# Kernel optimization log

Measured on AMD Instinct MI355X. Metric: run time of the kernel, lower is better.

Reference implementation:

```python
import jax, jax.numpy as jnp
import numpy as np
from math import sqrt

DIM = 64
N_HEADS = 12
B, T = 4, 2048


def setup_inputs() -> dict:
    key = jax.random.key(0)
    ks = jax.random.split(key, 5)
    scale = 1.0 / sqrt(DIM)
    x = jax.random.normal(ks[0], (B, T, DIM), dtype=jnp.float32)
    # torch Linear(dim, h*dim) weight is (h*dim, dim); store transposed (dim, h*dim)
    Wq = jax.random.uniform(ks[1], (DIM, N_HEADS * DIM), dtype=jnp.float32, minval=-scale, maxval=scale)
    Wk = jax.random.uniform(ks[2], (DIM, N_HEADS * DIM), dtype=jnp.float32, minval=-scale, maxval=scale)
    Wv = jax.random.uniform(ks[3], (DIM, N_HEADS * DIM), dtype=jnp.float32, minval=-scale, maxval=scale)
    # finalDense: Linear(h*dim, dim) -> stored (h*dim, dim)
    Wo = jax.random.uniform(ks[4], (N_HEADS * DIM, DIM), dtype=jnp.float32,
                            minval=-1.0 / sqrt(N_HEADS * DIM), maxval=1.0 / sqrt(N_HEADS * DIM))
    return {"x": x, "Wq": Wq, "Wk": Wk, "Wv": Wv, "Wo": Wo}


def reference(x, Wq, Wk, Wv, Wo):
    b, t, k = x.shape
    h = Wq.shape[1] // k
    # NOTE: the original module does .view(b,t,h,k).view(b*h,t,k), a flat
    # row-major memory reinterpretation (NOT a head transpose). jnp.reshape
    # is the same flat reshape, so this is faithful.
    Q = (x @ Wq).reshape(b * h, t, k)
    K = (x @ Wk).reshape(b * h, t, k)
    V = (x @ Wv).reshape(b * h, t, k)
    # W[b,i,j] = sum_k K[b,i,k] * Q[b,j,k], scaled; softmax over j (last dim)
    W = jnp.einsum('bik,bjk->bij', K, Q) / sqrt(k)
    W = jax.nn.softmax(W, axis=2)
    Z = jnp.einsum('bij,bjk->bik', W, V)  # (b*h, t, k)
    Z = Z.reshape(b, t, h * k)  # flat reinterpretation, matches torch views
    return Z @ Wo
```

## Files before the change

kernel.cpp:

```cpp
#include <hip/hip_runtime.h>
#include <hip/hip_bf16.h>


#define DIM 64
#define NH 12
#define HD 768
#define BT 8192
#define TSEQ 2048
#define NSLICE 48
#define SLICE (TSEQ*DIM)

#define LDQ 72
#define LDT 72
#define LDP 72

typedef unsigned short ushort;
typedef __attribute__((ext_vector_type(8))) short bf16x8;
typedef __attribute__((ext_vector_type(4))) short bf16x4;
typedef __attribute__((ext_vector_type(4))) float f32x4;
typedef __attribute__((ext_vector_type(16))) float f32x16;
typedef __attribute__((ext_vector_type(4))) unsigned int uint32x4;

#define SCALE2 0.18033688011112042f

__device__ __forceinline__ ushort f2b(float f) {
    union { float f; unsigned int i; } v; v.f = f;
    unsigned int x = v.i;
    return (ushort)((x + 0x7fffu + ((x >> 16) & 1u)) >> 16);
}

__global__ __launch_bounds__(256) void prep_w(
    const float* __restrict__ Wq, const float* __restrict__ Wk,
    const float* __restrict__ Wv, const float* __restrict__ Wo,
    ushort* __restrict__ Wt, ushort* __restrict__ Wot)
{
    __shared__ float tile[64][65];
    int bx = blockIdx.x;
    int z = bx / 12, bt = bx % 12;
    const float* __restrict__ IN = (z == 0) ? Wq : (z == 1) ? Wk : (z == 2) ? Wv : Wo;
    int inStride  = (z < 3) ? HD : DIM;
    int outStride = (z < 3) ? DIM : HD;
    int rbase = (z < 3) ? 0 : bt * 64;
    int cbase = (z < 3) ? bt * 64 : 0;
    ushort* __restrict__ OUT = (z < 3) ? (Wt + (size_t)z * HD * DIM) : Wot;
    int t = threadIdx.x;
    int r = t >> 2, c0 = (t & 3) * 16;
    #pragma unroll
    for (int cc = 0; cc < 16; cc += 4) {
        float4 a = *(const float4*)&IN[(size_t)(rbase + r) * inStride + cbase + c0 + cc];
        tile[r][c0 + cc] = a.x; tile[r][c0 + cc + 1] = a.y;
        tile[r][c0 + cc + 2] = a.z; tile[r][c0 + cc + 3] = a.w;
    }
    __syncthreads();
    int cl = t >> 2, r0 = (t & 3) * 16;
    ushort tmp[16] __attribute__((aligned(16)));
    #pragma unroll
    for (int rr = 0; rr < 16; ++rr) tmp[rr] = f2b(tile[r0 + rr][cl]);
    *(float4*)&OUT[(size_t)(cbase + cl) * outStride + rbase + r0] = *(const float4*)tmp;
    *(float4*)&OUT[(size_t)(cbase + cl) * outStride + rbase + r0 + 8] = *(const float4*)&tmp[8];
}

__global__ __launch_bounds__(256) void qkv_kernel(
    const float* __restrict__ x, const ushort* __restrict__ Wt,
    ushort* __restrict__ Q, ushort* __restrict__ K, ushort* __restrict__ V)
{
    int rt = blockIdx.x, yg = blockIdx.y;
    int t = threadIdx.x, w = t >> 6, lane = t & 63;
    int ln = lane & 15, q = lane >> 4;
    int m0 = rt * 64 + w * 16;

    float4 xa = *(const float4*)&x[(size_t)(m0 + ln) * DIM + q * 8];
    float4 xb_ = *(const float4*)&x[(size_t)(m0 + ln) * DIM + q * 8 + 4];
    float4 xc = *(const float4*)&x[(size_t)(m0 + ln) * DIM + 32 + q * 8];
    float4 xd = *(const float4*)&x[(size_t)(m0 + ln) * DIM + 32 + q * 8 + 4];
    ushort ta[8] __attribute__((aligned(16)));
    ushort tb[8] __attribute__((aligned(16)));
    ta[0]=f2b(xa.x); ta[1]=f2b(xa.y); ta[2]=f2b(xa.z); ta[3]=f2b(xa.w);
    ta[4]=f2b(xb_.x); ta[5]=f2b(xb_.y); ta[6]=f2b(xb_.z); ta[7]=f2b(xb_.w);
    tb[0]=f2b(xc.x); tb[1]=f2b(xc.y); tb[2]=f2b(xc.z); tb[3]=f2b(xc.w);
    tb[4]=f2b(xd.x); tb[5]=f2b(xd.y); tb[6]=f2b(xd.z); tb[7]=f2b(xd.w);
    bf16x8 af0 = *(const bf16x8*)ta;
    bf16x8 af1 = *(const bf16x8*)tb;

    for (int cc = 0; cc < 6; ++cc) {
        int ct = yg * 6 + cc;
        int which = ct / 12;
        int col0 = (ct % 12) * 64;
        const ushort* __restrict__ Wz = Wt + (size_t)which * HD * DIM;
        ushort* __restrict__ Y = (which == 0) ? Q : (which == 1) ? K : V;
        float sc = (which == 0) ? SCALE2 : 1.f;
        #pragma unroll
        for (int nt = 0; nt < 4; ++nt) {
            int n = col0 + nt * 16 + ln;
            bf16x8 bf0 = *(const bf16x8*)&Wz[(size_t)n * DIM + q * 8];
            bf16x8 bf1 = *(const bf16x8*)&Wz[(size_t)n * DIM + 32 + q * 8];
            f32x4 acc = (f32x4){0.f, 0.f, 0.f, 0.f};
            acc = __builtin_amdgcn_mfma_f32_16x16x32_bf16(af0, bf0, acc, 0, 0, 0);
            acc = __builtin_amdgcn_mfma_f32_16x16x32_bf16(af1, bf1, acc, 0, 0, 0);
            #pragma unroll
            for (int r = 0; r < 4; ++r)
                Y[(size_t)(m0 + q * 4 + r) * HD + col0 + nt * 16 + ln] = f2b(acc[r] * sc);
        }
    }
}

__global__ __launch_bounds__(256) void vtrans_kernel(
    const ushort* __restrict__ V, ushort* __restrict__ Vt)
{
    __shared__ ushort tileT[64 * LDT];
    int tt = blockIdx.x, s = blockIdx.y;
    const ushort* __restrict__ Vp = V + (size_t)s * SLICE;
    ushort* __restrict__ Vo = Vt + (size_t)s * SLICE;
    int t = threadIdx.x;
    int r = t >> 3, c = (t & 7) * 8;
    ushort va[8] __attribute__((aligned(16)));
    ushort vb[8] __attribute__((aligned(16)));
    *(float4*)va = *(const float4*)&Vp[(size_t)(tt * 64 + r) * DIM + c];
    *(float4*)vb = *(const float4*)&Vp[(size_t)(tt * 64 + r + 32) * DIM + c];
    int g0 = ((r >> 3) ^ (c >> 3)) * 8 + (r & 7);
    int g1 = (((r + 32) >> 3) ^ (c >> 3)) * 8 + (r & 7);
    #pragma unroll
    for (int k = 0; k < 8; ++k) {
        tileT[(c + k) * LDT + g0] = va[k];
        tileT[(c + k) * LDT + g1] = vb[k];
    }
    __syncthreads();
    #pragma unroll
    for (int j = 0; j < 2; ++j) {
        int flat = t + 256 * j;
        int d = flat >> 3, tg = flat & 7;
        int sg = tg ^ ((d >> 3) & 7);
        float4 vv = *(const float4*)&tileT[d * LDT + sg * 8];
        *(float4*)&Vo[(size_t)d * TSEQ + tt * 64 + tg * 8] = vv;
    }
}

__global__ __launch_bounds__(256, 3) void attn_kernel(
    const ushort* __restrict__ Qs, const ushort* __restrict__ Ks,
    const ushort* __restrict__ Vts, ushort* __restrict__ Zs)
{
    __shared__ ushort sh[4 * 64 * LDQ];
    int itile = blockIdx.x, s = blockIdx.y;
    const ushort* __restrict__ Qp = Qs + (size_t)s * SLICE;
    const ushort* __restrict__ Kp = Ks + (size_t)s * SLICE;
    const ushort* __restrict__ Vp = Vts + (size_t)s * SLICE;
    ushort* __restrict__ Zp = Zs + (size_t)s * SLICE;
    int t = threadIdx.x, w = t >> 6, lane = t & 63;
    int i5 = lane & 31, hi = lane >> 5;

    bf16x8 kf[4];
    {
        size_t krow = (size_t)(itile * 128 + w * 32 + i5) * DIM;
        #pragma unroll
        for (int c = 0; c < 4; ++c)
            kf[c] = *(const bf16x8*)&Kp[krow + c * 16 + hi * 8];
    }

    f32x16 Of0, Of1;
    #pragma unroll
    for (int r = 0; r < 16; ++r) { Of0[r] = 0.f; Of1[r] = 0.f; }
    float lsum = 0.f;

    int sr = t >> 3, sc = (t & 7) * 8;
    const ushort* qsrc0 = &Qp[(size_t)sr * DIM + sc];
    const ushort* qsrc1 = &Qp[(size_t)(sr + 32) * DIM + sc];
    const ushort* vsrc0 = &Vp[(size_t)sr * TSEQ + sc];
    const ushort* vsrc1 = &Vp[(size_t)(sr + 32) * TSEQ + sc];

    float4 qa0 = *(const float4*)qsrc0;
    float4 qa1 = *(const float4*)qsrc1;
    float4 va0 = *(const float4*)vsrc0;
    float4 va1 = *(const float4*)vsrc1;
    *(float4*)&sh[sr * LDQ + sc] = qa0;
    *(float4*)&sh[(sr + 32) * LDQ + sc] = qa1;
    *(float4*)&sh[2 * 64 * LDQ + sr * LDQ + sc] = va0;
    *(float4*)&sh[2 * 64 * LDQ + (sr + 32) * LDQ + sc] = va1;
    qa0 = *(const float4*)(qsrc0 + 64 * DIM);
    qa1 = *(const float4*)(qsrc1 + 64 * DIM);
    va0 = *(const float4*)(vsrc0 + 64);
    va1 = *(const float4*)(vsrc1 + 64);
    __syncthreads();

    for (int tt = 0; tt < 32; ++tt) {
        int ib = tt & 1;
        const ushort* Qc = sh + ib * (64 * LDQ);
        const ushort* Vc = sh + (2 + ib) * (64 * LDQ);
        if (tt < 31) {
            ushort* Qn = sh + (ib ^ 1) * (64 * LDQ);
            ushort* Vn = sh + (2 + (ib ^ 1)) * (64 * LDQ);
            *(float4*)&Qn[sr * LDQ + sc] = qa0;
            *(float4*)&Qn[(sr + 32) * LDQ + sc] = qa1;
            *(float4*)&Vn[sr * LDQ + sc] = va0;
            *(float4*)&Vn[(sr + 32) * LDQ + sc] = va1;
            if (tt < 30) {
                size_t qo = (size_t)(tt + 2) * 64 * DIM;
                int vo = (tt + 2) * 64;
                qa0 = *(const float4*)(qsrc0 + qo);
                qa1 = *(const float4*)(qsrc1 + qo);
                va0 = *(const float4*)(vsrc0 + vo);
                va1 = *(const float4*)(vsrc1 + vo);
            }
        }
        #pragma unroll
        for (int js = 0; js < 2; ++js) {
            f32x16 acc;
            #pragma unroll
            for (int r = 0; r < 16; ++r) acc[r] = 0.f;
            #pragma unroll
            for (int c = 0; c < 4; ++c) {
                bf16x8 aQ = *(const bf16x8*)&Qc[(js * 32 + i5) * LDQ + c * 16 + hi * 8];
                acc = __builtin_amdgcn_mfma_f32_32x32x16_bf16(aQ, kf[c], acc, 0, 0, 0);
            }
            unsigned wv[8];
            float ls = 0.f;
            #pragma unroll
            for (int k = 0; k < 8; ++k) {
                float p0 = __builtin_amdgcn_exp2f(acc[2 * k]);
                float p1 = __builtin_amdgcn_exp2f(acc[2 * k + 1]);
                unsigned int b0 = __float_as_uint(p0), b1 = __float_as_uint(p1);
                unsigned int t1 = b1 & 0xFFFF0000u;
                unsigned int h = (b0 >> 16) | t1;
                ls += __uint_as_float(h << 16) + __uint_as_float(t1);
                wv[k] = h;
            }
            lsum += ls;
            uint32x4 u0 = { wv[0], wv[1], wv[2], wv[3] };
            uint32x4 u1 = { wv[4], wv[5], wv[6], wv[7] };
            bf16x8 pa0 = __builtin_bit_cast(bf16x8, u0);
            bf16x8 pa1 = __builtin_bit_cast(bf16x8, u1);
            #pragma unroll
            for (int dt = 0; dt < 2; ++dt) {
                int vbase = (dt * 32 + i5) * LDQ + js * 32 + 4 * hi;
                bf16x4 v0a = *(const bf16x4*)&Vc[vbase];
                bf16x4 v0b = *(const bf16x4*)&Vc[vbase + 8];
                bf16x4 v1a = *(const bf16x4*)&Vc[vbase + 16];
                bf16x4 v1b = *(const bf16x4*)&Vc[vbase + 24];
                bf16x8 vb0 = __builtin_shufflevector(v0a, v0b, 0, 1, 2, 3, 4, 5, 6, 7);
                bf16x8 vb1 = __builtin_shufflevector(v1a, v1b, 0, 1, 2, 3, 4, 5, 6, 7);
                if (dt == 0) {
                    Of0 = __builtin_amdgcn_mfma_f32_32x32x16_bf16(pa0, vb0, Of0, 0, 0, 0);
                    Of0 = __builtin_amdgcn_mfma_f32_32x32x16_bf16(pa1, vb1, Of0, 0, 0, 0);
                } else {
                    Of1 = __builtin_amdgcn_mfma_f32_32x32x16_bf16(pa0, vb0, Of1, 0, 0, 0);
                    Of1 = __builtin_amdgcn_mfma_f32_32x32x16_bf16(pa1, vb1, Of1, 0, 0, 0);
                }
            }
        }
        __syncthreads();
    }

    float l = lsum + __shfl_xor(lsum, 32);
    float linv = 1.f / l;
    #pragma unroll
    for (int r = 0; r < 16; ++r) {
        int cr = (r & 3) + 8 * (r >> 2);
        float li = __shfl(linv, cr + 4 * hi);
        int row = w * 32 + cr + 4 * hi;
        sh[row * LDQ + i5]      = f2b(Of0[r] * li);
        sh[row * LDQ + 32 + i5] = f2b(Of1[r] * li);
    }
    __syncthreads();
    int zr = t >> 1, zc = (t & 1) * 32;
    size_t zoff = (size_t)(itile * 128 + zr) * DIM + zc;
    #pragma unroll
    for (int c4 = 0; c4 < 4; ++c4)
        *(float4*)&Zp[zoff + c4 * 8] = *(const float4*)&sh[zr * LDQ + zc + c4 * 8];
}

__global__ __launch_bounds__(64) void out_kernel(
    const ushort* __restrict__ Z, const ushort* __restrict__ Wot,
    float* __restrict__ out)
{
    int m0 = blockIdx.x * 32;
    int lane = threadIdx.x;
    int ln = lane & 15, q = lane >> 4;
    f32x4 acc[2][4];
    #pragma unroll
    for (int u = 0; u < 2; ++u)
        #pragma unroll
        for (int nt = 0; nt < 4; ++nt) acc[u][nt] = (f32x4){0.f, 0.f, 0.f, 0.f};
    for (int kc = 0; kc < 24; ++kc) {
        bf16x8 a0 = *(const bf16x8*)&Z[(size_t)(m0 + ln) * HD + kc * 32 + q * 8];
        bf16x8 a1 = *(const bf16x8*)&Z[(size_t)(m0 + 16 + ln) * HD + kc * 32 + q * 8];
        #pragma unroll
        for (int nt = 0; nt < 4; ++nt) {
            bf16x8 bf = *(const bf16x8*)&Wot[(size_t)(nt * 16 + ln) * HD + kc * 32 + q * 8];
            acc[0][nt] = __builtin_amdgcn_mfma_f32_16x16x32_bf16(a0, bf, acc[0][nt], 0, 0, 0);
            acc[1][nt] = __builtin_amdgcn_mfma_f32_16x16x32_bf16(a1, bf, acc[1][nt], 0, 0, 0);
        }
    }
    #pragma unroll
    for (int u = 0; u < 2; ++u)
        #pragma unroll
        for (int nt = 0; nt < 4; ++nt)
            #pragma unroll
            for (int r = 0; r < 4; ++r)
                out[(size_t)(m0 + u * 16 + q * 4 + r) * DIM + nt * 16 + ln] = acc[u][nt][r];
}

extern "C" void kernel_launch(void* const* d_in, const int* in_sizes, int n_in,
                              void* d_out, int out_size, void* d_ws, size_t ws_size,
                              hipStream_t stream)
{
    const float* x  = (const float*)d_in[0];
    const float* Wq = (const float*)d_in[1];
    const float* Wk = (const float*)d_in[2];
    const float* Wv = (const float*)d_in[3];
    const float* Wo = (const float*)d_in[4];
    float* out = (float*)d_out;

    const size_t n = (size_t)BT * HD;
    ushort* Q   = (ushort*)d_ws;
    ushort* K   = Q + n;
    ushort* V   = K + n;
    ushort* Vt  = V + n;
    ushort* Wt  = Vt;
    ushort* Wot = Vt + n;
    ushort* Z   = V;

    prep_w<<<48, 256, 0, stream>>>(Wq, Wk, Wv, Wo, Wt, Wot);
    qkv_kernel<<<dim3(128, 6), 256, 0, stream>>>(x, Wt, Q, K, V);
    vtrans_kernel<<<dim3(32, 48), 256, 0, stream>>>(V, Vt);
    attn_kernel<<<dim3(16, 48), 256, 0, stream>>>(Q, K, Vt, Z);
    out_kernel<<<256, 64, 0, stream>>>(Z, Wot, out);
}
```

Before: 173.5 us.

## Swizzle attention LDS tiles and restructure output projection into 4-wave blocks

```diff
diff --git a/kernel.cpp b/kernel.cpp
--- a/kernel.cpp
+++ b/kernel.cpp
@@ -12,7 +12,8 @@
 
 #define LDQ 72
 #define LDT 72
-#define LDP 72
+
+#define SWZ(r, c) ((r) * LDQ + (((((c) >> 3) - 2 * (r)) & 7) << 3) + ((c) & 7))
 
 typedef unsigned short ushort;
 typedef __attribute__((ext_vector_type(8))) short bf16x8;
@@ -171,10 +172,14 @@
     float4 qa1 = *(const float4*)qsrc1;
     float4 va0 = *(const float4*)vsrc0;
     float4 va1 = *(const float4*)vsrc1;
-    *(float4*)&sh[sr * LDQ + sc] = qa0;
-    *(float4*)&sh[(sr + 32) * LDQ + sc] = qa1;
-    *(float4*)&sh[2 * 64 * LDQ + sr * LDQ + sc] = va0;
-    *(float4*)&sh[2 * 64 * LDQ + (sr + 32) * LDQ + sc] = va1;
+    {
+        ushort* Q0 = sh;
+        ushort* V0 = sh + 2 * 64 * LDQ;
+        *(float4*)&Q0[SWZ(sr, sc)] = qa0;
+        *(float4*)&Q0[SWZ(sr + 32, sc)] = qa1;
+        *(float4*)&V0[SWZ(sr, sc)] = va0;
+        *(float4*)&V0[SWZ(sr + 32, sc)] = va1;
+    }
     qa0 = *(const float4*)(qsrc0 + 64 * DIM);
     qa1 = *(const float4*)(qsrc1 + 64 * DIM);
     va0 = *(const float4*)(vsrc0 + 64);
@@ -188,10 +193,10 @@
         if (tt < 31) {
             ushort* Qn = sh + (ib ^ 1) * (64 * LDQ);
             ushort* Vn = sh + (2 + (ib ^ 1)) * (64 * LDQ);
-            *(float4*)&Qn[sr * LDQ + sc] = qa0;
-            *(float4*)&Qn[(sr + 32) * LDQ + sc] = qa1;
-            *(float4*)&Vn[sr * LDQ + sc] = va0;
-            *(float4*)&Vn[(sr + 32) * LDQ + sc] = va1;
+            *(float4*)&Qn[SWZ(sr, sc)] = qa0;
+            *(float4*)&Qn[SWZ(sr + 32, sc)] = qa1;
+            *(float4*)&Vn[SWZ(sr, sc)] = va0;
+            *(float4*)&Vn[SWZ(sr + 32, sc)] = va1;
             if (tt < 30) {
                 size_t qo = (size_t)(tt + 2) * 64 * DIM;
                 int vo = (tt + 2) * 64;
@@ -208,7 +213,7 @@
             for (int r = 0; r < 16; ++r) acc[r] = 0.f;
             #pragma unroll
             for (int c = 0; c < 4; ++c) {
-                bf16x8 aQ = *(const bf16x8*)&Qc[(js * 32 + i5) * LDQ + c * 16 + hi * 8];
+                bf16x8 aQ = *(const bf16x8*)&Qc[SWZ(js * 32 + i5, c * 16 + hi * 8)];
                 acc = __builtin_amdgcn_mfma_f32_32x32x16_bf16(aQ, kf[c], acc, 0, 0, 0);
             }
             unsigned wv[8];
@@ -230,11 +235,12 @@
             bf16x8 pa1 = __builtin_bit_cast(bf16x8, u1);
             #pragma unroll
             for (int dt = 0; dt < 2; ++dt) {
-                int vbase = (dt * 32 + i5) * LDQ + js * 32 + 4 * hi;
-                bf16x4 v0a = *(const bf16x4*)&Vc[vbase];
-                bf16x4 v0b = *(const bf16x4*)&Vc[vbase + 8];
-                bf16x4 v1a = *(const bf16x4*)&Vc[vbase + 16];
-                bf16x4 v1b = *(const bf16x4*)&Vc[vbase + 24];
+                int vr = dt * 32 + i5;
+                int uc = js * 32 + 4 * hi;
+                bf16x4 v0a = *(const bf16x4*)&Vc[SWZ(vr, uc)];
+                bf16x4 v0b = *(const bf16x4*)&Vc[SWZ(vr, uc + 8)];
+                bf16x4 v1a = *(const bf16x4*)&Vc[SWZ(vr, uc + 16)];
+                bf16x4 v1b = *(const bf16x4*)&Vc[SWZ(vr, uc + 24)];
                 bf16x8 vb0 = __builtin_shufflevector(v0a, v0b, 0, 1, 2, 3, 4, 5, 6, 7);
                 bf16x8 vb1 = __builtin_shufflevector(v1a, v1b, 0, 1, 2, 3, 4, 5, 6, 7);
                 if (dt == 0) {
@@ -256,46 +262,40 @@
         int cr = (r & 3) + 8 * (r >> 2);
         float li = __shfl(linv, cr + 4 * hi);
         int row = w * 32 + cr + 4 * hi;
-        sh[row * LDQ + i5]      = f2b(Of0[r] * li);
-        sh[row * LDQ + 32 + i5] = f2b(Of1[r] * li);
+        sh[SWZ(row, i5)]      = f2b(Of0[r] * li);
+        sh[SWZ(row, 32 + i5)] = f2b(Of1[r] * li);
     }
     __syncthreads();
     int zr = t >> 1, zc = (t & 1) * 32;
     size_t zoff = (size_t)(itile * 128 + zr) * DIM + zc;
     #pragma unroll
     for (int c4 = 0; c4 < 4; ++c4)
-        *(float4*)&Zp[zoff + c4 * 8] = *(const float4*)&sh[zr * LDQ + zc + c4 * 8];
-}
-
-__global__ __launch_bounds__(64) void out_kernel(
+        *(float4*)&Zp[zoff + c4 * 8] = *(const float4*)&sh[SWZ(zr, zc + c4 * 8)];
+}
+
+__global__ __launch_bounds__(256) void out_kernel(
     const ushort* __restrict__ Z, const ushort* __restrict__ Wot,
     float* __restrict__ out)
 {
-    int m0 = blockIdx.x * 32;
-    int lane = threadIdx.x;
+    int t = threadIdx.x, w = t >> 6, lane = t & 63;
+    int m0 = blockIdx.x * 64 + w * 16;
     int ln = lane & 15, q = lane >> 4;
-    f32x4 acc[2][4];
-    #pragma unroll
-    for (int u = 0; u < 2; ++u)
-        #pragma unroll
-        for (int nt = 0; nt < 4; ++nt) acc[u][nt] = (f32x4){0.f, 0.f, 0.f, 0.f};
+    f32x4 acc[4];
+    #pragma unroll
+    for (int nt = 0; nt < 4; ++nt) acc[nt] = (f32x4){0.f, 0.f, 0.f, 0.f};
     for (int kc = 0; kc < 24; ++kc) {
-        bf16x8 a0 = *(const bf16x8*)&Z[(size_t)(m0 + ln) * HD + kc * 32 + q * 8];
-        bf16x8 a1 = *(const bf16x8*)&Z[(size_t)(m0 + 16 + ln) * HD + kc * 32 + q * 8];
+        bf16x8 a = *(const bf16x8*)&Z[(size_t)(m0 + ln) * HD + kc * 32 + q * 8];
         #pragma unroll
         for (int nt = 0; nt < 4; ++nt) {
             bf16x8 bf = *(const bf16x8*)&Wot[(size_t)(nt * 16 + ln) * HD + kc * 32 + q * 8];
-            acc[0][nt] = __builtin_amdgcn_mfma_f32_16x16x32_bf16(a0, bf, acc[0][nt], 0, 0, 0);
-            acc[1][nt] = __builtin_amdgcn_mfma_f32_16x16x32_bf16(a1, bf, acc[1][nt], 0, 0, 0);
+            acc[nt] = __builtin_amdgcn_mfma_f32_16x16x32_bf16(a, bf, acc[nt], 0, 0, 0);
         }
     }
     #pragma unroll
-    for (int u = 0; u < 2; ++u)
-        #pragma unroll
-        for (int nt = 0; nt < 4; ++nt)
-            #pragma unroll
-            for (int r = 0; r < 4; ++r)
-                out[(size_t)(m0 + u * 16 + q * 4 + r) * DIM + nt * 16 + ln] = acc[u][nt][r];
+    for (int nt = 0; nt < 4; ++nt)
+        #pragma unroll
+        for (int r = 0; r < 4; ++r)
+            out[(size_t)(m0 + q * 4 + r) * DIM + nt * 16 + ln] = acc[nt][r];
 }
 
 extern "C" void kernel_launch(void* const* d_in, const int* in_sizes, int n_in,
@@ -322,5 +322,5 @@
     qkv_kernel<<<dim3(128, 6), 256, 0, stream>>>(x, Wt, Q, K, V);
     vtrans_kernel<<<dim3(32, 48), 256, 0, stream>>>(V, Vt);
     attn_kernel<<<dim3(16, 48), 256, 0, stream>>>(Q, K, Vt, Z);
-    out_kernel<<<256, 64, 0, stream>>>(Z, Wot, out);
-}
+    out_kernel<<<128, 256, 0, stream>>>(Z, Wot, out);
+}
```

Result: slower. 179.9 us (+3.7%).

## Fuse V transpose into attention LDS staging and drop vtrans kernel

Applied to the files above, without the earlier changes.

```diff
diff --git a/kernel.cpp b/kernel.cpp
--- a/kernel.cpp
+++ b/kernel.cpp
@@ -11,8 +11,6 @@
 #define SLICE (TSEQ*DIM)
 
 #define LDQ 72
-#define LDT 72
-#define LDP 72
 
 typedef unsigned short ushort;
 typedef __attribute__((ext_vector_type(8))) short bf16x8;
@@ -64,7 +62,7 @@
     const float* __restrict__ x, const ushort* __restrict__ Wt,
     ushort* __restrict__ Q, ushort* __restrict__ K, ushort* __restrict__ V)
 {
-    int rt = blockIdx.x, yg = blockIdx.y;
+    int rt = blockIdx.x, half = blockIdx.y;
     int t = threadIdx.x, w = t >> 6, lane = t & 63;
     int ln = lane & 15, q = lane >> 4;
     int m0 = rt * 64 + w * 16;
@@ -82,8 +80,8 @@
     bf16x8 af0 = *(const bf16x8*)ta;
     bf16x8 af1 = *(const bf16x8*)tb;
 
-    for (int cc = 0; cc < 6; ++cc) {
-        int ct = yg * 6 + cc;
+    for (int cc = 0; cc < 18; ++cc) {
+        int ct = half * 18 + cc;
         int which = ct / 12;
         int col0 = (ct % 12) * 64;
         const ushort* __restrict__ Wz = Wt + (size_t)which * HD * DIM;
@@ -104,46 +102,15 @@
     }
 }
 
-__global__ __launch_bounds__(256) void vtrans_kernel(
-    const ushort* __restrict__ V, ushort* __restrict__ Vt)
-{
-    __shared__ ushort tileT[64 * LDT];
-    int tt = blockIdx.x, s = blockIdx.y;
-    const ushort* __restrict__ Vp = V + (size_t)s * SLICE;
-    ushort* __restrict__ Vo = Vt + (size_t)s * SLICE;
-    int t = threadIdx.x;
-    int r = t >> 3, c = (t & 7) * 8;
-    ushort va[8] __attribute__((aligned(16)));
-    ushort vb[8] __attribute__((aligned(16)));
-    *(float4*)va = *(const float4*)&Vp[(size_t)(tt * 64 + r) * DIM + c];
-    *(float4*)vb = *(const float4*)&Vp[(size_t)(tt * 64 + r + 32) * DIM + c];
-    int g0 = ((r >> 3) ^ (c >> 3)) * 8 + (r & 7);
-    int g1 = (((r + 32) >> 3) ^ (c >> 3)) * 8 + (r & 7);
-    #pragma unroll
-    for (int k = 0; k < 8; ++k) {
-        tileT[(c + k) * LDT + g0] = va[k];
-        tileT[(c + k) * LDT + g1] = vb[k];
-    }
-    __syncthreads();
-    #pragma unroll
-    for (int j = 0; j < 2; ++j) {
-        int flat = t + 256 * j;
-        int d = flat >> 3, tg = flat & 7;
-        int sg = tg ^ ((d >> 3) & 7);
-        float4 vv = *(const float4*)&tileT[d * LDT + sg * 8];
-        *(float4*)&Vo[(size_t)d * TSEQ + tt * 64 + tg * 8] = vv;
-    }
-}
-
 __global__ __launch_bounds__(256, 3) void attn_kernel(
     const ushort* __restrict__ Qs, const ushort* __restrict__ Ks,
-    const ushort* __restrict__ Vts, ushort* __restrict__ Zs)
+    const ushort* __restrict__ Vs, ushort* __restrict__ Zs)
 {
     __shared__ ushort sh[4 * 64 * LDQ];
     int itile = blockIdx.x, s = blockIdx.y;
     const ushort* __restrict__ Qp = Qs + (size_t)s * SLICE;
     const ushort* __restrict__ Kp = Ks + (size_t)s * SLICE;
-    const ushort* __restrict__ Vp = Vts + (size_t)s * SLICE;
+    const ushort* __restrict__ Vp = Vs + (size_t)s * SLICE;
     ushort* __restrict__ Zp = Zs + (size_t)s * SLICE;
     int t = threadIdx.x, w = t >> 6, lane = t & 63;
     int i5 = lane & 31, hi = lane >> 5;
@@ -164,21 +131,32 @@
     int sr = t >> 3, sc = (t & 7) * 8;
     const ushort* qsrc0 = &Qp[(size_t)sr * DIM + sc];
     const ushort* qsrc1 = &Qp[(size_t)(sr + 32) * DIM + sc];
-    const ushort* vsrc0 = &Vp[(size_t)sr * TSEQ + sc];
-    const ushort* vsrc1 = &Vp[(size_t)(sr + 32) * TSEQ + sc];
+    const ushort* vsrc0 = &Vp[(size_t)sr * DIM + sc];
+    const ushort* vsrc1 = &Vp[(size_t)(sr + 32) * DIM + sc];
+    int b0 = (((sr >> 3) ^ (sc >> 3)) << 3) + (sr & 7);
+    int b1 = ((((sr >> 3) + 4) ^ (sc >> 3)) << 3) + (sr & 7);
 
     float4 qa0 = *(const float4*)qsrc0;
     float4 qa1 = *(const float4*)qsrc1;
     float4 va0 = *(const float4*)vsrc0;
     float4 va1 = *(const float4*)vsrc1;
-    *(float4*)&sh[sr * LDQ + sc] = qa0;
-    *(float4*)&sh[(sr + 32) * LDQ + sc] = qa1;
-    *(float4*)&sh[2 * 64 * LDQ + sr * LDQ + sc] = va0;
-    *(float4*)&sh[2 * 64 * LDQ + (sr + 32) * LDQ + sc] = va1;
+    {
+        ushort* V0 = sh + 2 * 64 * LDQ;
+        *(float4*)&sh[sr * LDQ + sc] = qa0;
+        *(float4*)&sh[(sr + 32) * LDQ + sc] = qa1;
+        ushort u0[8] __attribute__((aligned(16)));
+        ushort u1[8] __attribute__((aligned(16)));
+        *(float4*)u0 = va0; *(float4*)u1 = va1;
+        #pragma unroll
+        for (int k = 0; k < 8; ++k) {
+            V0[(sc + k) * LDQ + b0] = u0[k];
+            V0[(sc + k) * LDQ + b1] = u1[k];
+        }
+    }
     qa0 = *(const float4*)(qsrc0 + 64 * DIM);
     qa1 = *(const float4*)(qsrc1 + 64 * DIM);
-    va0 = *(const float4*)(vsrc0 + 64);
-    va1 = *(const float4*)(vsrc1 + 64);
+    va0 = *(const float4*)(vsrc0 + 64 * DIM);
+    va1 = *(const float4*)(vsrc1 + 64 * DIM);
     __syncthreads();
 
     for (int tt = 0; tt < 32; ++tt) {
@@ -190,15 +168,20 @@
             ushort* Vn = sh + (2 + (ib ^ 1)) * (64 * LDQ);
             *(float4*)&Qn[sr * LDQ + sc] = qa0;
             *(float4*)&Qn[(sr + 32) * LDQ + sc] = qa1;
-            *(float4*)&Vn[sr * LDQ + sc] = va0;
-            *(float4*)&Vn[(sr + 32) * LDQ + sc] = va1;
+            ushort u0[8] __attribute__((aligned(16)));
+            ushort u1[8] __attribute__((aligned(16)));
+            *(float4*)u0 = va0; *(float4*)u1 = va1;
+            #pragma unroll
+            for (int k = 0; k < 8; ++k) {
+                Vn[(sc + k) * LDQ + b0] = u0[k];
+                Vn[(sc + k) * LDQ + b1] = u1[k];
+            }
             if (tt < 30) {
                 size_t qo = (size_t)(tt + 2) * 64 * DIM;
-                int vo = (tt + 2) * 64;
                 qa0 = *(const float4*)(qsrc0 + qo);
                 qa1 = *(const float4*)(qsrc1 + qo);
-                va0 = *(const float4*)(vsrc0 + vo);
-                va1 = *(const float4*)(vsrc1 + vo);
+                va0 = *(const float4*)(vsrc0 + qo);
+                va1 = *(const float4*)(vsrc1 + qo);
             }
         }
         #pragma unroll
@@ -217,9 +200,9 @@
             for (int k = 0; k < 8; ++k) {
                 float p0 = __builtin_amdgcn_exp2f(acc[2 * k]);
                 float p1 = __builtin_amdgcn_exp2f(acc[2 * k + 1]);
-                unsigned int b0 = __float_as_uint(p0), b1 = __float_as_uint(p1);
-                unsigned int t1 = b1 & 0xFFFF0000u;
-                unsigned int h = (b0 >> 16) | t1;
+                unsigned int bb0 = __float_as_uint(p0), bb1 = __float_as_uint(p1);
+                unsigned int t1 = bb1 & 0xFFFF0000u;
+                unsigned int h = (bb0 >> 16) | t1;
                 ls += __uint_as_float(h << 16) + __uint_as_float(t1);
                 wv[k] = h;
             }
@@ -230,11 +213,13 @@
             bf16x8 pa1 = __builtin_bit_cast(bf16x8, u1);
             #pragma unroll
             for (int dt = 0; dt < 2; ++dt) {
-                int vbase = (dt * 32 + i5) * LDQ + js * 32 + 4 * hi;
-                bf16x4 v0a = *(const bf16x4*)&Vc[vbase];
-                bf16x4 v0b = *(const bf16x4*)&Vc[vbase + 8];
-                bf16x4 v1a = *(const bf16x4*)&Vc[vbase + 16];
-                bf16x4 v1b = *(const bf16x4*)&Vc[vbase + 24];
+                int d = dt * 32 + i5;
+                int dh = d >> 3;
+                int rowb = d * LDQ + 4 * hi;
+                bf16x4 v0a = *(const bf16x4*)&Vc[rowb + (((js * 4 + 0) ^ dh) << 3)];
+                bf16x4 v0b = *(const bf16x4*)&Vc[rowb + (((js * 4 + 1) ^ dh) << 3)];
+                bf16x4 v1a = *(const bf16x4*)&Vc[rowb + (((js * 4 + 2) ^ dh) << 3)];
+                bf16x4 v1b = *(const bf16x4*)&Vc[rowb + (((js * 4 + 3) ^ dh) << 3)];
                 bf16x8 vb0 = __builtin_shufflevector(v0a, v0b, 0, 1, 2, 3, 4, 5, 6, 7);
                 bf16x8 vb1 = __builtin_shufflevector(v1a, v1b, 0, 1, 2, 3, 4, 5, 6, 7);
                 if (dt == 0) {
@@ -313,14 +298,12 @@
     ushort* Q   = (ushort*)d_ws;
     ushort* K   = Q + n;
     ushort* V   = K + n;
-    ushort* Vt  = V + n;
-    ushort* Wt  = Vt;
-    ushort* Wot = Vt + n;
-    ushort* Z   = V;
+    ushort* Z   = V + n;
+    ushort* Wt  = Z + n;
+    ushort* Wot = Wt + 3 * HD * DIM;
 
     prep_w<<<48, 256, 0, stream>>>(Wq, Wk, Wv, Wo, Wt, Wot);
-    qkv_kernel<<<dim3(128, 6), 256, 0, stream>>>(x, Wt, Q, K, V);
-    vtrans_kernel<<<dim3(32, 48), 256, 0, stream>>>(V, Vt);
-    attn_kernel<<<dim3(16, 48), 256, 0, stream>>>(Q, K, Vt, Z);
+    qkv_kernel<<<dim3(128, 2), 256, 0, stream>>>(x, Wt, Q, K, V);
+    attn_kernel<<<dim3(16, 48), 256, 0, stream>>>(Q, K, V, Z);
     out_kernel<<<256, 64, 0, stream>>>(Z, Wot, out);
 }
```

Result: slower. 183.4 us (+5.7%).

## Prefetch next weight tile in QKV projection and remap attention blocks per XCD

Applied to the files above, without the earlier changes.

```diff
diff --git a/kernel.cpp b/kernel.cpp
--- a/kernel.cpp
+++ b/kernel.cpp
@@ -12,7 +12,6 @@
 
 #define LDQ 72
 #define LDT 72
-#define LDP 72
 
 typedef unsigned short ushort;
 typedef __attribute__((ext_vector_type(8))) short bf16x8;
@@ -82,21 +81,44 @@
     bf16x8 af0 = *(const bf16x8*)ta;
     bf16x8 af1 = *(const bf16x8*)tb;
 
+    bf16x8 bf[8];
+    {
+        int ct0 = yg * 6;
+        const ushort* __restrict__ Wz0 = Wt + (size_t)(ct0 / 12) * HD * DIM;
+        int c0 = (ct0 % 12) * 64;
+        #pragma unroll
+        for (int nt = 0; nt < 4; ++nt) {
+            int n = c0 + nt * 16 + ln;
+            bf[2 * nt]     = *(const bf16x8*)&Wz0[(size_t)n * DIM + q * 8];
+            bf[2 * nt + 1] = *(const bf16x8*)&Wz0[(size_t)n * DIM + 32 + q * 8];
+        }
+    }
+
     for (int cc = 0; cc < 6; ++cc) {
         int ct = yg * 6 + cc;
         int which = ct / 12;
         int col0 = (ct % 12) * 64;
-        const ushort* __restrict__ Wz = Wt + (size_t)which * HD * DIM;
         ushort* __restrict__ Y = (which == 0) ? Q : (which == 1) ? K : V;
         float sc = (which == 0) ? SCALE2 : 1.f;
+        bf16x8 cur[8];
+        #pragma unroll
+        for (int i = 0; i < 8; ++i) cur[i] = bf[i];
+        if (cc < 5) {
+            int ct2 = ct + 1;
+            const ushort* __restrict__ Wz2 = Wt + (size_t)(ct2 / 12) * HD * DIM;
+            int col2 = (ct2 % 12) * 64;
+            #pragma unroll
+            for (int nt = 0; nt < 4; ++nt) {
+                int n = col2 + nt * 16 + ln;
+                bf[2 * nt]     = *(const bf16x8*)&Wz2[(size_t)n * DIM + q * 8];
+                bf[2 * nt + 1] = *(const bf16x8*)&Wz2[(size_t)n * DIM + 32 + q * 8];
+            }
+        }
         #pragma unroll
         for (int nt = 0; nt < 4; ++nt) {
-            int n = col0 + nt * 16 + ln;
-            bf16x8 bf0 = *(const bf16x8*)&Wz[(size_t)n * DIM + q * 8];
-            bf16x8 bf1 = *(const bf16x8*)&Wz[(size_t)n * DIM + 32 + q * 8];
             f32x4 acc = (f32x4){0.f, 0.f, 0.f, 0.f};
-            acc = __builtin_amdgcn_mfma_f32_16x16x32_bf16(af0, bf0, acc, 0, 0, 0);
-            acc = __builtin_amdgcn_mfma_f32_16x16x32_bf16(af1, bf1, acc, 0, 0, 0);
+            acc = __builtin_amdgcn_mfma_f32_16x16x32_bf16(af0, cur[2 * nt], acc, 0, 0, 0);
+            acc = __builtin_amdgcn_mfma_f32_16x16x32_bf16(af1, cur[2 * nt + 1], acc, 0, 0, 0);
             #pragma unroll
             for (int r = 0; r < 4; ++r)
                 Y[(size_t)(m0 + q * 4 + r) * HD + col0 + nt * 16 + ln] = f2b(acc[r] * sc);
@@ -140,7 +162,10 @@
     const ushort* __restrict__ Vts, ushort* __restrict__ Zs)
 {
     __shared__ ushort sh[4 * 64 * LDQ];
-    int itile = blockIdx.x, s = blockIdx.y;
+    int bid = blockIdx.x + (blockIdx.y << 4);
+    int xcd = bid & 7, idx = bid >> 3;
+    int s = xcd * 6 + idx % 6;
+    int itile = idx / 6;
     const ushort* __restrict__ Qp = Qs + (size_t)s * SLICE;
     const ushort* __restrict__ Kp = Ks + (size_t)s * SLICE;
     const ushort* __restrict__ Vp = Vts + (size_t)s * SLICE;
```

Result: slower. 179.4 us (+3.4%).
